# Performance work log

Measured on AMD Instinct MI355X. Metric: run time of the kernel, lower is better.

Reference implementation:

```python
import jax, jax.numpy as jnp
import numpy as np

VOCAB, EMBED, HIDDEN = 32000, 128, 128
LN_EPS = 1e-5
NEG = -1e30

def _layernorm(x, w, b):
    m = jnp.mean(x, axis=-1, keepdims=True)
    v = jnp.mean((x - m) ** 2, axis=-1, keepdims=True)
    return (x - m) * jax.lax.rsqrt(v + LN_EPS) * w + b

def _encode(ids, mask, emb, W1, b1, W2, b2, lnw, lnb):
    x = emb[ids]                                   # [B, L, EMBED]
    h = _layernorm(jax.nn.relu(x @ W1 + b1), lnw, lnb)
    h = _layernorm(jax.nn.relu(h @ W2 + b2), lnw, lnb)  # extra layer (num_layers=2)
    return h * mask[..., None].astype(h.dtype)

def setup_inputs() -> dict:
    key = jax.random.key(0)
    ks = jax.random.split(key, 16)
    s_emb = 1.0
    s_lin = 1.0 / np.sqrt(HIDDEN)
    def lin(k1, k2, din, dout):
        return (jax.random.uniform(k1, (din, dout), jnp.float32, -s_lin, s_lin),
                jax.random.uniform(k2, (dout,), jnp.float32, -s_lin, s_lin))
    q_emb = jax.random.normal(ks[0], (VOCAB, EMBED), jnp.float32).at[0].set(0.0)
    d_emb = jax.random.normal(ks[1], (VOCAB, EMBED), jnp.float32).at[0].set(0.0)
    qW1, qb1 = lin(ks[2], ks[3], EMBED, HIDDEN)
    qW2, qb2 = lin(ks[4], ks[5], HIDDEN, HIDDEN)
    dW1, db1 = lin(ks[6], ks[7], EMBED, HIDDEN)
    dW2, db2 = lin(ks[8], ks[9], HIDDEN, HIDDEN)
    q_lnw = jnp.ones((HIDDEN,), jnp.float32); q_lnb = jnp.zeros((HIDDEN,), jnp.float32)
    d_lnw = jnp.ones((HIDDEN,), jnp.float32); d_lnb = jnp.zeros((HIDDEN,), jnp.float32)
    query_ids = jax.random.randint(ks[10], (64, 64), 0, VOCAB, jnp.int32)
    doc_ids = jax.random.randint(ks[11], (64, 4096), 0, VOCAB, jnp.int32)
    query_mask = jnp.ones((64, 64), jnp.int32)
    doc_mask = jnp.ones((64, 4096), jnp.int32)
    return dict(query_ids=query_ids, doc_ids=doc_ids, query_mask=query_mask, doc_mask=doc_mask,
                q_emb=q_emb, qW1=qW1, qb1=qb1, qW2=qW2, qb2=qb2, q_lnw=q_lnw, q_lnb=q_lnb,
                d_emb=d_emb, dW1=dW1, db1=db1, dW2=dW2, db2=db2, d_lnw=d_lnw, d_lnb=d_lnb)

def reference(query_ids, doc_ids, query_mask, doc_mask,
              q_emb, qW1, qb1, qW2, qb2, q_lnw, q_lnb,
              d_emb, dW1, db1, dW2, db2, d_lnw, d_lnb):
    qv = _encode(query_ids, query_mask, q_emb, qW1, qb1, qW2, qb2, q_lnw, q_lnb)  # [B,Q,H]
    dv = _encode(doc_ids, doc_mask, d_emb, dW1, db1, dW2, db2, d_lnw, d_lnb)      # [B,D,H]
    sim = jnp.einsum('bqh,bdh->bqd', qv, dv)
    sim = sim + (1.0 - doc_mask[:, None, :].astype(sim.dtype)) * NEG
    return jnp.max(sim, axis=2).sum(axis=1)  # [B]
```

## Files before the change

### kernel.cpp

```cpp
#include <hip/hip_runtime.h>

typedef _Float16 f16;
typedef __attribute__((ext_vector_type(8))) _Float16 f16x8;
typedef __attribute__((ext_vector_type(4))) float f32x4;

#define XS 136
#define NEGV (-1e30f)


__device__ __forceinline__ void emb_to_xs(const float* __restrict__ row_src,
                                          f16* Xs, int myrow, int seg) {
  const float4* src = (const float4*)(row_src + seg * 32);
  f16x8* dst = (f16x8*)(Xs + myrow * XS + seg * 32);
#pragma unroll
  for (int i = 0; i < 4; ++i) {
    float4 v0 = src[2 * i], v1 = src[2 * i + 1];
    f16x8 o;
    o[0] = (f16)v0.x; o[1] = (f16)v0.y; o[2] = (f16)v0.z; o[3] = (f16)v0.w;
    o[4] = (f16)v1.x; o[5] = (f16)v1.y; o[6] = (f16)v1.z; o[7] = (f16)v1.w;
    dst[i] = o;
  }
}

__device__ __forceinline__ void load_afrag(f16x8* afrag, const f16* Xs,
                                           int wave, int lane) {
  const int r = lane & 15, quad = lane >> 4;
#pragma unroll
  for (int k = 0; k < 4; ++k)
    afrag[k] = *(const f16x8*)(Xs + (wave * 16 + r) * XS + quad * 8 + k * 32);
}

__device__ __forceinline__ void layer_mfma_inline(f32x4* acc, const f16x8* afrag,
                                                  const float* __restrict__ W,
                                                  int lane) {
  const int r = lane & 15, quad = lane >> 4;
#pragma unroll
  for (int nt = 0; nt < 8; ++nt) {
    f32x4 c = {0.f, 0.f, 0.f, 0.f};
#pragma unroll
    for (int k = 0; k < 4; ++k) {
      const float* src = W + (k * 32 + quad * 8) * 128 + nt * 16 + r;
      f16x8 b;
#pragma unroll
      for (int j = 0; j < 8; ++j) b[j] = (f16)src[j * 128];
      c = __builtin_amdgcn_mfma_f32_16x16x32_f16(afrag[k], b, c, 0, 0, 0);
    }
    acc[nt] = c;
  }
}

__device__ __forceinline__ void epilogue_ln(f32x4* acc, int wave, int lane, f16* Xs,
                                            const float* __restrict__ bias,
                                            const float* __restrict__ lnw,
                                            const float* __restrict__ lnb) {
  const int r = lane & 15, quad = lane >> 4;
  float s1[4] = {0, 0, 0, 0}, s2[4] = {0, 0, 0, 0};
#pragma unroll
  for (int nt = 0; nt < 8; ++nt) {
    float bv = bias[nt * 16 + r];
#pragma unroll
    for (int g = 0; g < 4; ++g) {
      float z = fmaxf(acc[nt][g] + bv, 0.f);
      acc[nt][g] = z; s1[g] += z; s2[g] += z * z;
    }
  }
#pragma unroll
  for (int off = 1; off < 16; off <<= 1) {
#pragma unroll
    for (int g = 0; g < 4; ++g) {
      s1[g] += __shfl_xor(s1[g], off);
      s2[g] += __shfl_xor(s2[g], off);
    }
  }
  float mean[4], rstd[4];
#pragma unroll
  for (int g = 0; g < 4; ++g) {
    mean[g] = s1[g] * (1.f / 128.f);
    rstd[g] = rsqrtf(s2[g] * (1.f / 128.f) - mean[g] * mean[g] + 1e-5f);
  }
#pragma unroll
  for (int nt = 0; nt < 8; ++nt) {
    float w = lnw[nt * 16 + r], bb = lnb[nt * 16 + r];
#pragma unroll
    for (int g = 0; g < 4; ++g) {
      float h = (acc[nt][g] - mean[g]) * rstd[g] * w + bb;
      Xs[(wave * 16 + quad * 4 + g) * XS + nt * 16 + r] = (f16)h;
    }
  }
}


__global__ __launch_bounds__(256) void encode_kernel(
    const int* __restrict__ qids, const int* __restrict__ qmask,
    const float* __restrict__ q_emb, const float* __restrict__ d_emb,
    const float* __restrict__ qW1, const float* __restrict__ qb1,
    const float* __restrict__ qW2, const float* __restrict__ qb2,
    const float* __restrict__ q_lnw, const float* __restrict__ q_lnb,
    const float* __restrict__ dW1, const float* __restrict__ db1,
    const float* __restrict__ dW2, const float* __restrict__ db2,
    const float* __restrict__ d_lnw, const float* __restrict__ d_lnb,
    f16* __restrict__ qv, f16* __restrict__ dvt) {
  __shared__ __align__(16) f16 Xs[64 * XS];
  const int tid = threadIdx.x, wave = tid >> 6, lane = tid & 63;
  const int myrow = tid >> 2, seg = tid & 3;
  f32x4 acc[8];
  f16x8 afrag[4];
  if (blockIdx.x < 500) {
    const int v0 = blockIdx.x * 64;
    emb_to_xs(d_emb + (size_t)(v0 + myrow) * 128, Xs, myrow, seg);
    load_afrag(afrag, Xs, wave, lane);
    layer_mfma_inline(acc, afrag, dW1, lane);
    epilogue_ln(acc, wave, lane, Xs, db1, d_lnw, d_lnb);
    load_afrag(afrag, Xs, wave, lane);
    layer_mfma_inline(acc, afrag, dW2, lane);
    epilogue_ln(acc, wave, lane, Xs, db2, d_lnw, d_lnb);
    f16x8* dst = (f16x8*)(dvt + (size_t)(v0 + myrow) * 128 + seg * 32);
    const f16x8* src = (const f16x8*)(Xs + myrow * XS + seg * 32);
#pragma unroll
    for (int i = 0; i < 4; ++i) dst[i] = src[i];
    return;
  }
  const int b = blockIdx.x - 500;
  emb_to_xs(q_emb + (size_t)qids[b * 64 + myrow] * 128, Xs, myrow, seg);
  load_afrag(afrag, Xs, wave, lane);
  layer_mfma_inline(acc, afrag, qW1, lane);
  epilogue_ln(acc, wave, lane, Xs, qb1, q_lnw, q_lnb);
  load_afrag(afrag, Xs, wave, lane);
  layer_mfma_inline(acc, afrag, qW2, lane);
  epilogue_ln(acc, wave, lane, Xs, qb2, q_lnw, q_lnb);
  __syncthreads();
#pragma unroll
  for (int i = 0; i < 4; ++i) {
    int u = tid + i * 256;
    int r = u & 15, quad = (u >> 4) & 3, k = (u >> 6) & 3, mt = u >> 8;
    int row = mt * 16 + r;
    f16 m = (f16)(float)qmask[b * 64 + row];
    f16x8 v = *(const f16x8*)(Xs + row * XS + k * 32 + quad * 8);
#pragma unroll
    for (int j = 0; j < 8; ++j) v[j] = v[j] * m;
    *(f16x8*)(qv + (size_t)b * 8192 + (size_t)u * 8) = v;
  }
}

__global__ __launch_bounds__(256) void docsim_kernel(
    const int* __restrict__ dids, const int* __restrict__ dmask,
    const f16* __restrict__ dvt, const f16* __restrict__ qv,
    float* __restrict__ partials) {
  __shared__ __align__(16) f16 Xs[64 * XS];
  const int tid = threadIdx.x, wave = tid >> 6, lane = tid & 63;
  const int b = blockIdx.x >> 4;
  const int dc0 = (blockIdx.x & 15) * 4;
  const int myrow = tid >> 2, seg = tid & 3;
  const int r = lane & 15, quad = lane >> 4;
  f16x8 qfrag[4];
#pragma unroll
  for (int k = 0; k < 4; ++k) {
    int u = (wave * 4 + k) * 64 + quad * 16 + r;
    qfrag[k] = *(const f16x8*)(qv + (size_t)b * 8192 + (size_t)u * 8);
  }
  int myid[4];
#pragma unroll
  for (int c = 0; c < 4; ++c)
    myid[c] = dids[(size_t)b * 4096 + (dc0 + c) * 64 + myrow];
#pragma unroll
  for (int c = 0; c < 4; ++c) {
    const int dc = dc0 + c;
    float mv[4];
#pragma unroll
    for (int nt = 0; nt < 4; ++nt)
      mv[nt] = (float)dmask[(size_t)b * 4096 + dc * 64 + nt * 16 + r];
    f16x8 row[4];
    {
      const f16x8* src = (const f16x8*)(dvt + (size_t)myid[c] * 128 + seg * 32);
#pragma unroll
      for (int i = 0; i < 4; ++i) row[i] = src[i];
    }
    if (c) __syncthreads();
    {
      f16x8* dst = (f16x8*)(Xs + myrow * XS + seg * 32);
#pragma unroll
      for (int i = 0; i < 4; ++i) dst[i] = row[i];
    }
    __syncthreads();
    float rowmax[4] = {NEGV, NEGV, NEGV, NEGV};
#pragma unroll
    for (int nt = 0; nt < 4; ++nt) {
      f32x4 cc = {0.f, 0.f, 0.f, 0.f};
#pragma unroll
      for (int k = 0; k < 4; ++k) {
        f16x8 bfrag = *(const f16x8*)(Xs + (nt * 16 + r) * XS + quad * 8 + k * 32);
        cc = __builtin_amdgcn_mfma_f32_16x16x32_f16(qfrag[k], bfrag, cc, 0, 0, 0);
      }
#pragma unroll
      for (int g = 0; g < 4; ++g) {
        float v = (mv[nt] != 0.f) ? cc[g] : NEGV;
        rowmax[g] = fmaxf(rowmax[g], v);
      }
    }
#pragma unroll
    for (int off = 1; off < 16; off <<= 1) {
#pragma unroll
      for (int g = 0; g < 4; ++g)
        rowmax[g] = fmaxf(rowmax[g], __shfl_xor(rowmax[g], off));
    }
    if (r == 0) {
#pragma unroll
      for (int g = 0; g < 4; ++g) {
        int q = wave * 16 + quad * 4 + g;
        partials[((size_t)b * 64 + q) * 64 + dc] = rowmax[g];
      }
    }
  }
}

__global__ __launch_bounds__(256) void reduce_kernel(
    const float* __restrict__ partials, float* __restrict__ out) {
  __shared__ float red[64][4];
  const int b = blockIdx.x, tid = threadIdx.x;
  const int q = tid >> 2, seg = tid & 3;
  const float4* p = (const float4*)(partials + ((size_t)b * 64 + q) * 64 + seg * 16);
  float m = NEGV;
#pragma unroll
  for (int i = 0; i < 4; ++i) {
    float4 v = p[i];
    m = fmaxf(m, fmaxf(fmaxf(v.x, v.y), fmaxf(v.z, v.w)));
  }
  red[q][seg] = m;
  __syncthreads();
  if (tid < 64) {
    float qm = fmaxf(fmaxf(red[tid][0], red[tid][1]), fmaxf(red[tid][2], red[tid][3]));
    float s = qm;
#pragma unroll
    for (int off = 1; off < 64; off <<= 1) s += __shfl_xor(s, off);
    if (tid == 0) out[b] = s;
  }
}


extern "C" void kernel_launch(void* const* d_in, const int* in_sizes, int n_in,
                              void* d_out, int out_size, void* d_ws, size_t ws_size,
                              hipStream_t stream) {
  const int* query_ids  = (const int*)d_in[0];
  const int* doc_ids    = (const int*)d_in[1];
  const int* query_mask = (const int*)d_in[2];
  const int* doc_mask   = (const int*)d_in[3];
  const float* q_emb = (const float*)d_in[4];
  const float* qW1 = (const float*)d_in[5];
  const float* qb1 = (const float*)d_in[6];
  const float* qW2 = (const float*)d_in[7];
  const float* qb2 = (const float*)d_in[8];
  const float* q_lnw = (const float*)d_in[9];
  const float* q_lnb = (const float*)d_in[10];
  const float* d_emb = (const float*)d_in[11];
  const float* dW1 = (const float*)d_in[12];
  const float* db1 = (const float*)d_in[13];
  const float* dW2 = (const float*)d_in[14];
  const float* db2 = (const float*)d_in[15];
  const float* d_lnw = (const float*)d_in[16];
  const float* d_lnb = (const float*)d_in[17];

  char* ws = (char*)d_ws;
  f16* dvt = (f16*)(ws + 0);
  f16* qv  = (f16*)(ws + 8192000);
  float* partials = (float*)(ws + 8192000 + 1048576);
  float* out = (float*)d_out;

  encode_kernel<<<564, 256, 0, stream>>>(query_ids, query_mask, q_emb, d_emb,
                                         qW1, qb1, qW2, qb2, q_lnw, q_lnb,
                                         dW1, db1, dW2, db2, d_lnw, d_lnb,
                                         qv, dvt);
  docsim_kernel<<<1024, 256, 0, stream>>>(doc_ids, doc_mask, dvt, qv, partials);
  reduce_kernel<<<64, 256, 0, stream>>>(partials, out);
}
```

Before: 149.7 us.

## Pre-convert weights to fp16 fragment layout and stage them into LDS via global_load_lds

A new prep kernel converts the four weight matrices to fp16, pre-swizzled into the MFMA B-fragment order. The encode kernel then copies each weight matrix into shared memory with direct global-to-LDS loads and reads fragments from LDS. This replaces the old per-lane strided fp32 global gathers and conversions, and the layer-2 weight load now overlaps the layer-1 epilogue. In exchange it adds an extra kernel launch, 32KB more LDS per block (which can lower occupancy), and extra barriers.

New measurement: 134.5 us. 10.2% less time.

```diff
diff --git a/kernel.cpp b/kernel.cpp
--- a/kernel.cpp
+++ b/kernel.cpp
@@ -7,6 +7,21 @@
 #define XS 136
 #define NEGV (-1e30f)
 
+
+__device__ __forceinline__ void gl_lds16(const f16* g, f16* l) {
+  __builtin_amdgcn_global_load_lds(
+      (const __attribute__((address_space(1))) unsigned int*)(g),
+      (__attribute__((address_space(3))) unsigned int*)(l), 16, 0, 0);
+}
+
+__device__ __forceinline__ void stage_w_full(const f16* __restrict__ Wf,
+                                             f16* Ws, int wave, int lane) {
+#pragma unroll
+  for (int c = 0; c < 8; ++c) {
+    int chunk = wave * 8 + c;
+    gl_lds16(Wf + chunk * 512 + lane * 8, Ws + chunk * 512);
+  }
+}
 
 __device__ __forceinline__ void emb_to_xs(const float* __restrict__ row_src,
                                           f16* Xs, int myrow, int seg) {
@@ -30,19 +45,15 @@
     afrag[k] = *(const f16x8*)(Xs + (wave * 16 + r) * XS + quad * 8 + k * 32);
 }
 
-__device__ __forceinline__ void layer_mfma_inline(f32x4* acc, const f16x8* afrag,
-                                                  const float* __restrict__ W,
-                                                  int lane) {
-  const int r = lane & 15, quad = lane >> 4;
+__device__ __forceinline__ void layer_mfma_lds(f32x4* acc, const f16x8* afrag,
+                                               const f16* Ws, int lane) {
+  const f16* Wl = Ws + lane * 8;
 #pragma unroll
   for (int nt = 0; nt < 8; ++nt) {
     f32x4 c = {0.f, 0.f, 0.f, 0.f};
 #pragma unroll
     for (int k = 0; k < 4; ++k) {
-      const float* src = W + (k * 32 + quad * 8) * 128 + nt * 16 + r;
-      f16x8 b;
-#pragma unroll
-      for (int j = 0; j < 8; ++j) b[j] = (f16)src[j * 128];
+      f16x8 b = *(const f16x8*)(Wl + (nt * 4 + k) * 512);
       c = __builtin_amdgcn_mfma_f32_16x16x32_f16(afrag[k], b, c, 0, 0, 0);
     }
     acc[nt] = c;
@@ -90,44 +101,69 @@
 }
 
 
+__global__ __launch_bounds__(256) void prep_kernel(
+    const float* __restrict__ qW1, const float* __restrict__ qW2,
+    const float* __restrict__ dW1, const float* __restrict__ dW2,
+    f16* __restrict__ out) {
+  int mat = blockIdx.x >> 3;
+  int blk = blockIdx.x & 7;
+  const float* W = mat == 0 ? qW1 : mat == 1 ? qW2 : mat == 2 ? dW1 : dW2;
+  int u = blk * 256 + threadIdx.x;
+  int r = u & 15, quad = (u >> 4) & 3, k = (u >> 6) & 3, nt = u >> 8;
+  const float* src = W + (k * 32 + quad * 8) * 128 + nt * 16 + r;
+  f16x8 o;
+#pragma unroll
+  for (int j = 0; j < 8; ++j) o[j] = (f16)src[j * 128];
+  *(f16x8*)(out + (size_t)mat * 16384 + (size_t)u * 8) = o;
+}
+
 __global__ __launch_bounds__(256) void encode_kernel(
     const int* __restrict__ qids, const int* __restrict__ qmask,
     const float* __restrict__ q_emb, const float* __restrict__ d_emb,
-    const float* __restrict__ qW1, const float* __restrict__ qb1,
-    const float* __restrict__ qW2, const float* __restrict__ qb2,
+    const f16* __restrict__ qW1f, const float* __restrict__ qb1,
+    const f16* __restrict__ qW2f, const float* __restrict__ qb2,
     const float* __restrict__ q_lnw, const float* __restrict__ q_lnb,
-    const float* __restrict__ dW1, const float* __restrict__ db1,
-    const float* __restrict__ dW2, const float* __restrict__ db2,
+    const f16* __restrict__ dW1f, const float* __restrict__ db1,
+    const f16* __restrict__ dW2f, const float* __restrict__ db2,
     const float* __restrict__ d_lnw, const float* __restrict__ d_lnb,
     f16* __restrict__ qv, f16* __restrict__ dvt) {
   __shared__ __align__(16) f16 Xs[64 * XS];
+  __shared__ __align__(16) f16 Ws[16384];
   const int tid = threadIdx.x, wave = tid >> 6, lane = tid & 63;
   const int myrow = tid >> 2, seg = tid & 3;
+  const bool dside = blockIdx.x < 500;
+  const int b = dside ? 0 : blockIdx.x - 500;
+  const int v0 = blockIdx.x * 64;
+
+  const f16* W1f = dside ? dW1f : qW1f;
+  const f16* W2f = dside ? dW2f : qW2f;
+  const float* b1 = dside ? db1 : qb1;
+  const float* b2 = dside ? db2 : qb2;
+  const float* lnw = dside ? d_lnw : q_lnw;
+  const float* lnb = dside ? d_lnb : q_lnb;
+
+  stage_w_full(W1f, Ws, wave, lane);
+  if (dside) emb_to_xs(d_emb + (size_t)(v0 + myrow) * 128, Xs, myrow, seg);
+  else       emb_to_xs(q_emb + (size_t)qids[b * 64 + myrow] * 128, Xs, myrow, seg);
+  __syncthreads();
   f32x4 acc[8];
   f16x8 afrag[4];
-  if (blockIdx.x < 500) {
-    const int v0 = blockIdx.x * 64;
-    emb_to_xs(d_emb + (size_t)(v0 + myrow) * 128, Xs, myrow, seg);
-    load_afrag(afrag, Xs, wave, lane);
-    layer_mfma_inline(acc, afrag, dW1, lane);
-    epilogue_ln(acc, wave, lane, Xs, db1, d_lnw, d_lnb);
-    load_afrag(afrag, Xs, wave, lane);
-    layer_mfma_inline(acc, afrag, dW2, lane);
-    epilogue_ln(acc, wave, lane, Xs, db2, d_lnw, d_lnb);
+  load_afrag(afrag, Xs, wave, lane);
+  layer_mfma_lds(acc, afrag, Ws, lane);
+  __syncthreads();
+  stage_w_full(W2f, Ws, wave, lane);
+  epilogue_ln(acc, wave, lane, Xs, b1, lnw, lnb);
+  __syncthreads();
+  load_afrag(afrag, Xs, wave, lane);
+  layer_mfma_lds(acc, afrag, Ws, lane);
+  epilogue_ln(acc, wave, lane, Xs, b2, lnw, lnb);
+  if (dside) {
     f16x8* dst = (f16x8*)(dvt + (size_t)(v0 + myrow) * 128 + seg * 32);
     const f16x8* src = (const f16x8*)(Xs + myrow * XS + seg * 32);
 #pragma unroll
     for (int i = 0; i < 4; ++i) dst[i] = src[i];
     return;
   }
-  const int b = blockIdx.x - 500;
-  emb_to_xs(q_emb + (size_t)qids[b * 64 + myrow] * 128, Xs, myrow, seg);
-  load_afrag(afrag, Xs, wave, lane);
-  layer_mfma_inline(acc, afrag, qW1, lane);
-  epilogue_ln(acc, wave, lane, Xs, qb1, q_lnw, q_lnb);
-  load_afrag(afrag, Xs, wave, lane);
-  layer_mfma_inline(acc, afrag, qW2, lane);
-  epilogue_ln(acc, wave, lane, Xs, qb2, q_lnw, q_lnb);
   __syncthreads();
 #pragma unroll
   for (int i = 0; i < 4; ++i) {
@@ -260,14 +296,20 @@
   const float* d_lnb = (const float*)d_in[17];
 
   char* ws = (char*)d_ws;
-  f16* dvt = (f16*)(ws + 0);
-  f16* qv  = (f16*)(ws + 8192000);
-  float* partials = (float*)(ws + 8192000 + 1048576);
+  f16* wts  = (f16*)(ws + 0);
+  f16* qW1f = wts;
+  f16* qW2f = wts + 16384;
+  f16* dW1f = wts + 32768;
+  f16* dW2f = wts + 49152;
+  f16* dvt = (f16*)(ws + 131072);
+  f16* qv  = (f16*)(ws + 131072 + 8192000);
+  float* partials = (float*)(ws + 131072 + 8192000 + 1048576);
   float* out = (float*)d_out;
 
+  prep_kernel<<<32, 256, 0, stream>>>(qW1, qW2, dW1, dW2, wts);
   encode_kernel<<<564, 256, 0, stream>>>(query_ids, query_mask, q_emb, d_emb,
-                                         qW1, qb1, qW2, qb2, q_lnw, q_lnb,
-                                         dW1, db1, dW2, db2, d_lnw, d_lnb,
+                                         qW1f, qb1, qW2f, qb2, q_lnw, q_lnb,
+                                         dW1f, db1, dW2f, db2, d_lnw, d_lnb,
                                          qv, dvt);
   docsim_kernel<<<1024, 256, 0, stream>>>(doc_ids, doc_mask, dvt, qv, partials);
   reduce_kernel<<<64, 256, 0, stream>>>(partials, out);
```
